# Kernel optimization log

Hardware: AMD Instinct MI355X
Metric: run time of the kernel (lower is better)

The kernel has to match this reference:

```python
import jax, jax.numpy as jnp
import numpy as np

# dims
B, W, L = 64, 64, 16          # sentences, words per sentence, max chars per word
E, H, V = 128, 512, 256       # char_embedding_size, word_embedding_size, char vocab


def setup_inputs() -> dict:
    key = jax.random.key(0)
    ks = jax.random.split(key, 8)
    chars = jax.random.randint(ks[0], (B, W, L), 1, V)          # char ids (0 = pad, unused in valid region)
    word_lens = jax.random.randint(ks[1], (B, W), 1, L + 1)     # per-word char counts in [1, L]
    emb = (jax.random.normal(ks[2], (V, E), jnp.float32) * 0.1).at[0].set(0.0)  # padding_idx=0 -> zero row

    def lstm_params(k):
        k1, k2, k3, k4 = jax.random.split(k, 4)
        s = 1.0 / np.sqrt(H)
        return (jax.random.uniform(k1, (4 * H, E), jnp.float32, -s, s),
                jax.random.uniform(k2, (4 * H, H), jnp.float32, -s, s),
                jax.random.uniform(k3, (4 * H,), jnp.float32, -s, s),
                jax.random.uniform(k4, (4 * H,), jnp.float32, -s, s))

    Wih_f, Whh_f, bih_f, bhh_f = lstm_params(ks[3])
    Wih_b, Whh_b, bih_b, bhh_b = lstm_params(ks[4])
    s = 1.0 / np.sqrt(2 * H)
    Wp = jax.random.uniform(ks[5], (H, 2 * H), jnp.float32, -s, s)
    bp = jax.random.uniform(ks[6], (H,), jnp.float32, -s, s)
    return dict(chars=chars, word_lens=word_lens, emb=emb,
                Wih_f=Wih_f, Whh_f=Whh_f, bih_f=bih_f, bhh_f=bhh_f,
                Wih_b=Wih_b, Whh_b=Whh_b, bih_b=bih_b, bhh_b=bhh_b,
                Wp=Wp, bp=bp)


def _lstm_last(x, lens, Wih, Whh, b):
    """Run a batched LSTM over x [N,L,E]; return hidden state at step lens-1 -> [N,H].
    PyTorch gate order: i, f, g, o."""
    N = x.shape[0]
    xw = jnp.einsum('nle,ge->nlg', x, Wih) + b  # [N, L, 4H], input projections precomputed

    def step(carry, xt):
        h, c = carry
        g = xt + h @ Whh.T
        i, f, gg, o = jnp.split(g, 4, axis=-1)
        c = jax.nn.sigmoid(f) * c + jax.nn.sigmoid(i) * jnp.tanh(gg)
        h = jax.nn.sigmoid(o) * jnp.tanh(c)
        return (h, c), h

    init = (jnp.zeros((N, H), x.dtype), jnp.zeros((N, H), x.dtype))
    _, hs = jax.lax.scan(step, init, jnp.swapaxes(xw, 0, 1))  # [L, N, H]
    hs = jnp.swapaxes(hs, 0, 1)                               # [N, L, H]
    idx = jnp.broadcast_to((lens - 1)[:, None, None], (N, 1, H))
    return jnp.take_along_axis(hs, idx, axis=1)[:, 0]


def reference(chars, word_lens, emb, Wih_f, Whh_f, bih_f, bhh_f,
              Wih_b, Whh_b, bih_b, bhh_b, Wp, bp):
    N = B * W
    lens = word_lens.reshape(N)
    x = emb[chars.reshape(N, L)]  # [N, L, E] char embeddings (dropout is identity in eval)

    # forward direction: hidden at last valid char (padded steps come after, don't matter)
    h_fwd = _lstm_last(x, lens, Wih_f, Whh_f, bih_f + bhh_f)

    # backward direction == forward LSTM over the length-aware reversed word,
    # taking hidden at step lens-1 (matches pack_sequence backward output at pos 0)
    t = jnp.arange(L)
    rev_idx = jnp.clip(lens[:, None] - 1 - t[None, :], 0, L - 1)  # [N, L]
    x_rev = jnp.take_along_axis(x, rev_idx[:, :, None], axis=1)
    h_bwd = _lstm_last(x_rev, lens, Wih_b, Whh_b, bih_b + bhh_b)

    concat = jnp.concatenate([h_bwd, h_fwd], axis=-1)  # torch order: (reverse, forward)
    out = concat @ Wp.T + bp                            # [N, H]
    return out.reshape(B, W, H)
```

## Files before the change

### kernel.cpp

```cpp
#include <hip/hip_runtime.h>

typedef unsigned short u16;
typedef __bf16 bf16x8 __attribute__((ext_vector_type(8)));
typedef float f32x4 __attribute__((ext_vector_type(4)));

#define NW 4096
#define HDIM 512
#define EDIM 128
#define G4 2048
#define LMAX 16
#define KREC 640

__device__ __forceinline__ u16 f2bf(float f) {
  unsigned u = __float_as_uint(f);
  u += 0x7FFFu + ((u >> 16) & 1u);
  return (u16)(u >> 16);
}

__device__ __forceinline__ float sigf(float x) { return 1.f / (1.f + __expf(-x)); }
__device__ __forceinline__ float tanha(float x) {
  float ax = fabsf(x);
  float e = __expf(2.f * ax);
  float t = 1.f - 2.f / (e + 1.f);
  return x < 0.f ? -t : t;
}

__device__ __forceinline__ void gload16(const void* g, void* l) {
  __builtin_amdgcn_global_load_lds((const __attribute__((address_space(1))) void*)g,
                                   (__attribute__((address_space(3))) void*)l, 16, 0, 0);
}

union V16 { int4 i; bf16x8 b; };
__device__ __forceinline__ bf16x8 ldfrag(const u16* p) {
  V16 v; v.i = *(const int4*)p; return v.b;
}

__global__ __launch_bounds__(256) void sort_kernel(
    const int* __restrict__ lens,
    int* __restrict__ perm, int* __restrict__ lens_s, int* __restrict__ nactive) {
  __shared__ int cnt[LMAX + 1];
  __shared__ int start[LMAX + 1];
  __shared__ int cursor[LMAX + 1];
  int tid = threadIdx.x;
  if (tid <= LMAX) cnt[tid] = 0;
  __syncthreads();
  for (int w = tid; w < NW; w += 256) atomicAdd(&cnt[lens[w]], 1);
  __syncthreads();
  if (tid == 0) {
    int acc = 0;
    for (int l = LMAX; l >= 1; --l) { start[l] = acc; acc += cnt[l]; }
    start[0] = acc;
  }
  __syncthreads();
  if (tid <= LMAX) cursor[tid] = start[tid];
  if (tid < LMAX) nactive[tid] = start[tid];
  __syncthreads();
  for (int w = tid; w < NW; w += 256) {
    int l = lens[w];
    int pos = atomicAdd(&cursor[l], 1);
    perm[pos] = w;
    lens_s[pos] = l;
  }
}

__global__ __launch_bounds__(256) void prep_kernel(
    const int* __restrict__ chars,
    const int* __restrict__ perm, const int* __restrict__ lens_s,
    const float* __restrict__ emb,
    const float* __restrict__ Wih_f, const float* __restrict__ Whh_f,
    const float* __restrict__ bih_f, const float* __restrict__ bhh_f,
    const float* __restrict__ Wih_b, const float* __restrict__ Whh_b,
    const float* __restrict__ bih_b, const float* __restrict__ bhh_b,
    const float* __restrict__ Wp,
    u16* __restrict__ Wcat, float* __restrict__ bcat, u16* __restrict__ Wpb,
    u16* __restrict__ Xf, u16* __restrict__ Xb) {
  int idx = blockIdx.x * 256 + threadIdx.x;
  if (idx < 327680) {
    int d = idx / (2048 * 80);
    int r = idx % (2048 * 80);
    int p = r / 80, c8 = r % 80;
    int unit = p >> 2, gate = p & 3;
    int orig = gate * 512 + unit;
    const float* Wih = d ? Wih_b : Wih_f;
    const float* Whh = d ? Whh_b : Whh_f;
    int k = c8 * 8;
    const float* src = (k < EDIM) ? (Wih + (size_t)orig * EDIM + k)
                                  : (Whh + (size_t)orig * HDIM + (k - EDIM));
    union { u16 u[8]; int4 v; } t;
#pragma unroll
    for (int j = 0; j < 8; ++j) t.u[j] = f2bf(src[j]);
    *(int4*)(Wcat + ((size_t)d * G4 + p) * KREC + k) = t.v;
  } else if (idx < 331776) {
    int r = idx - 327680;
    int d = r / G4, p = r % G4;
    int unit = p >> 2, gate = p & 3;
    int orig = gate * 512 + unit;
    bcat[d * G4 + p] = d ? (bih_b[orig] + bhh_b[orig]) : (bih_f[orig] + bhh_f[orig]);
  } else if (idx < 397312) {
    int r = idx - 331776;
    int row = r >> 7, c8 = r & 127;
    union { u16 u[8]; int4 v; } t;
#pragma unroll
    for (int j = 0; j < 8; ++j) t.u[j] = f2bf(Wp[(size_t)row * 1024 + c8 * 8 + j]);
    *(int4*)(Wpb + (size_t)row * 1024 + c8 * 8) = t.v;
  } else {
    int r = idx - 397312;
    int tw = r >> 4, e8 = (r & 15) * 8;
    int t = tw >> 12, s = tw & (NW - 1);
    int w = perm[s];
    int len = lens_s[s];
    int cf = chars[w * LMAX + t];
    int tb = len - 1 - t; if (tb < 0) tb = 0;
    int cb = chars[w * LMAX + tb];
    union { u16 u[8]; int4 v; } vf, vb;
#pragma unroll
    for (int j = 0; j < 8; ++j) {
      vf.u[j] = f2bf(emb[(size_t)cf * EDIM + e8 + j]);
      vb.u[j] = f2bf(emb[(size_t)cb * EDIM + e8 + j]);
    }
    size_t o = ((size_t)t * NW + s) * EDIM + e8;
    *(int4*)(Xf + o) = vf.v;
    *(int4*)(Xb + o) = vb.v;
  }
}

__global__ __launch_bounds__(256) void step_kernel(
    const u16* __restrict__ Wcat, const float* __restrict__ bcat,
    const u16* __restrict__ Xf, const u16* __restrict__ Xb,
    const u16* __restrict__ hprev, u16* __restrict__ hnext,
    float* __restrict__ cst, u16* __restrict__ concat,
    const int* __restrict__ perm, const int* __restrict__ lens_s,
    const int* __restrict__ nactive, int t, int nIter, int first) {
  const int w0 = blockIdx.x * 128;
  if (w0 >= nactive[t]) return;

  __shared__ u16 ldsA[128 * 64];
  __shared__ u16 ldsB[128 * 64];

  const int tid = threadIdx.x;
  const int lane = tid & 63;
  const int wid = tid >> 6;
  const int wm = wid >> 1, wn = wid & 1;
  const int dir = blockIdx.z;
  const int m0 = blockIdx.y * 128;

  const u16* Wd = Wcat + (size_t)dir * G4 * KREC;
  const u16* Xd = dir ? Xb : Xf;
  const u16* hpd = hprev + (size_t)dir * NW * HDIM;

  f32x4 acc[4][4];
#pragma unroll
  for (int i = 0; i < 4; ++i)
#pragma unroll
    for (int j = 0; j < 4; ++j) acc[i][j] = (f32x4){0.f, 0.f, 0.f, 0.f};

  const int srow = tid >> 3;
  const int c8 = tid & 7;

  for (int kit = 0; kit < nIter; ++kit) {
    const int k0 = kit * 64;
#pragma unroll
    for (int s = 0; s < 4; ++s) {
      int rr = s * 32 + srow;
      gload16(Wd + (size_t)(m0 + rr) * KREC + k0 + c8 * 8, ldsA + rr * 64 + c8 * 8);
    }
#pragma unroll
    for (int s = 0; s < 4; ++s) {
      int rr = s * 32 + srow;
      int word = w0 + rr;
      int k = k0 + c8 * 8;
      const u16* src = (k < EDIM) ? (Xd + ((size_t)t * NW + word) * EDIM + k)
                                  : (hpd + (size_t)word * HDIM + (k - EDIM));
      gload16(src, ldsB + rr * 64 + c8 * 8);
    }
    __syncthreads();
#pragma unroll
    for (int kk = 0; kk < 2; ++kk) {
      const int ko = kk * 32 + (lane >> 4) * 8;
      bf16x8 af[4], bfr[4];
#pragma unroll
      for (int mi = 0; mi < 4; ++mi)
        af[mi] = ldfrag(ldsA + (wm * 64 + mi * 16 + (lane & 15)) * 64 + ko);
#pragma unroll
      for (int ni = 0; ni < 4; ++ni)
        bfr[ni] = ldfrag(ldsB + (wn * 64 + ni * 16 + (lane & 15)) * 64 + ko);
#pragma unroll
      for (int mi = 0; mi < 4; ++mi)
#pragma unroll
        for (int ni = 0; ni < 4; ++ni)
          acc[mi][ni] = __builtin_amdgcn_mfma_f32_16x16x32_bf16(af[mi], bfr[ni], acc[mi][ni], 0, 0, 0);
    }
    __syncthreads();
  }

  const float* bcd = bcat + dir * G4;
  float* cd = cst + (size_t)dir * HDIM * NW;
  u16* hstage = ldsA;
#pragma unroll
  for (int mi = 0; mi < 4; ++mi) {
    int ul = wm * 16 + mi * 4 + (lane >> 4);
    int unit = blockIdx.y * 32 + ul;
    float4 bb = *(const float4*)(bcd + 4 * unit);
#pragma unroll
    for (int ni = 0; ni < 4; ++ni) {
      int wl = wn * 64 + ni * 16 + (lane & 15);
      int word = w0 + wl;
      f32x4 a = acc[mi][ni];
      float gi = a[0] + bb.x, gf = a[1] + bb.y, gg = a[2] + bb.z, go = a[3] + bb.w;
      size_t cidx = (size_t)unit * NW + word;
      float c0 = first ? 0.f : cd[cidx];
      float cn = sigf(gf) * c0 + sigf(gi) * tanha(gg);
      float hh = sigf(go) * tanha(cn);
      cd[cidx] = cn;
      hstage[wl * 32 + ul] = f2bf(hh);
    }
  }
  __syncthreads();

  u16* hnd = hnext + (size_t)dir * NW * HDIM;
  const int dirOff = dir ? 0 : HDIM;
#pragma unroll
  for (int r = 0; r < 2; ++r) {
    int i4 = tid * 2 + r;
    int wl = i4 >> 2, part = i4 & 3;
    int word = w0 + wl;
    int4 v = ((const int4*)hstage)[i4];
    *(int4*)(hnd + (size_t)word * HDIM + blockIdx.y * 32 + part * 8) = v;
    if (t == lens_s[word] - 1) {
      int orig = perm[word];
      *(int4*)(concat + (size_t)orig * 1024 + dirOff + blockIdx.y * 32 + part * 8) = v;
    }
  }
}

__global__ __launch_bounds__(256) void proj_kernel(
    const u16* __restrict__ concat, const u16* __restrict__ Wpb,
    const float* __restrict__ bp, float* __restrict__ out) {
  __shared__ u16 ldsA[128 * 64];
  __shared__ u16 ldsB[128 * 64];

  const int tid = threadIdx.x;
  const int lane = tid & 63;
  const int wid = tid >> 6;
  const int wm = wid >> 1, wn = wid & 1;
  const int m0 = blockIdx.x * 128;
  const int n0 = blockIdx.y * 128;

  f32x4 acc[4][4];
#pragma unroll
  for (int i = 0; i < 4; ++i)
#pragma unroll
    for (int j = 0; j < 4; ++j) acc[i][j] = (f32x4){0.f, 0.f, 0.f, 0.f};

  const int srow = tid >> 3;
  const int c8 = tid & 7;

  for (int kit = 0; kit < 16; ++kit) {
    const int k0 = kit * 64;
#pragma unroll
    for (int s = 0; s < 4; ++s) {
      int rr = s * 32 + srow;
      gload16(concat + (size_t)(m0 + rr) * 1024 + k0 + c8 * 8, ldsA + rr * 64 + c8 * 8);
      gload16(Wpb + (size_t)(n0 + rr) * 1024 + k0 + c8 * 8, ldsB + rr * 64 + c8 * 8);
    }
    __syncthreads();
#pragma unroll
    for (int kk = 0; kk < 2; ++kk) {
      const int ko = kk * 32 + (lane >> 4) * 8;
      bf16x8 af[4], bfr[4];
#pragma unroll
      for (int mi = 0; mi < 4; ++mi)
        af[mi] = ldfrag(ldsA + (wm * 64 + mi * 16 + (lane & 15)) * 64 + ko);
#pragma unroll
      for (int ni = 0; ni < 4; ++ni)
        bfr[ni] = ldfrag(ldsB + (wn * 64 + ni * 16 + (lane & 15)) * 64 + ko);
#pragma unroll
      for (int mi = 0; mi < 4; ++mi)
#pragma unroll
        for (int ni = 0; ni < 4; ++ni)
          acc[mi][ni] = __builtin_amdgcn_mfma_f32_16x16x32_bf16(af[mi], bfr[ni], acc[mi][ni], 0, 0, 0);
    }
    __syncthreads();
  }

  float bpv[4];
#pragma unroll
  for (int ni = 0; ni < 4; ++ni) bpv[ni] = bp[n0 + wn * 64 + ni * 16 + (lane & 15)];
#pragma unroll
  for (int mi = 0; mi < 4; ++mi)
#pragma unroll
    for (int ni = 0; ni < 4; ++ni)
#pragma unroll
      for (int rg = 0; rg < 4; ++rg) {
        int word = m0 + wm * 64 + mi * 16 + (lane >> 4) * 4 + rg;
        int hout = n0 + wn * 64 + ni * 16 + (lane & 15);
        out[(size_t)word * HDIM + hout] = acc[mi][ni][rg] + bpv[ni];
      }
}

extern "C" void kernel_launch(void* const* d_in, const int* in_sizes, int n_in,
                              void* d_out, int out_size, void* d_ws, size_t ws_size,
                              hipStream_t stream) {
  const int* chars = (const int*)d_in[0];
  const int* lens  = (const int*)d_in[1];
  const float* emb = (const float*)d_in[2];
  const float* Wih_f = (const float*)d_in[3];
  const float* Whh_f = (const float*)d_in[4];
  const float* bih_f = (const float*)d_in[5];
  const float* bhh_f = (const float*)d_in[6];
  const float* Wih_b = (const float*)d_in[7];
  const float* Whh_b = (const float*)d_in[8];
  const float* bih_b = (const float*)d_in[9];
  const float* bhh_b = (const float*)d_in[10];
  const float* Wp = (const float*)d_in[11];
  const float* bp = (const float*)d_in[12];
  float* out = (float*)d_out;

  char* ws = (char*)d_ws;
  size_t o = 0;
  u16* Wcat = (u16*)(ws + o);  o += (size_t)2 * G4 * KREC * 2;
  float* bcat = (float*)(ws + o); o += (size_t)2 * G4 * 4;
  u16* Wpb = (u16*)(ws + o);   o += (size_t)HDIM * 1024 * 2;
  u16* Xf = (u16*)(ws + o);    o += (size_t)LMAX * NW * EDIM * 2;
  u16* Xb = (u16*)(ws + o);    o += (size_t)LMAX * NW * EDIM * 2;
  u16* hbuf = (u16*)(ws + o);  o += (size_t)2 * 2 * NW * HDIM * 2;
  float* cst = (float*)(ws + o); o += (size_t)2 * HDIM * NW * 4;
  u16* concat = (u16*)(ws + o); o += (size_t)NW * 1024 * 2;
  int* perm = (int*)(ws + o);  o += (size_t)NW * 4;
  int* lens_s = (int*)(ws + o); o += (size_t)NW * 4;
  int* nactive = (int*)(ws + o); o += 64;

  sort_kernel<<<1, 256, 0, stream>>>(lens, perm, lens_s, nactive);

  prep_kernel<<<5648, 256, 0, stream>>>(chars, perm, lens_s, emb,
      Wih_f, Whh_f, bih_f, bhh_f, Wih_b, Whh_b, bih_b, bhh_b, Wp,
      Wcat, bcat, Wpb, Xf, Xb);

  const size_t hping = (size_t)2 * NW * HDIM;
  for (int t = 0; t < LMAX; ++t) {
    int ping = t & 1;
    u16* hprev = hbuf + (size_t)ping * hping;
    u16* hnext = hbuf + (size_t)(ping ^ 1) * hping;
    int nIter = (t == 0) ? 2 : 10;
    step_kernel<<<dim3(32, 16, 2), 256, 0, stream>>>(
        Wcat, bcat, Xf, Xb, hprev, hnext, cst, concat,
        perm, lens_s, nactive, t, nIter, t == 0 ? 1 : 0);
  }

  proj_kernel<<<dim3(32, 4), 256, 0, stream>>>(concat, Wpb, bp, out);
}
```

Measured before the change: 851.3 us.

## Swizzle global bf16 layouts for conflict-free LDS reads and double-buffer step GEMM

Weights, embeddings, hidden states and concat are now stored with an XOR swizzle of 16-byte chunks keyed on the row index. Because the direct-to-LDS copies preserve that order, the MFMA fragment reads from LDS hit different banks instead of conflicting. The step kernel also double-buffers its LDS tiles, so the next K-slice loads while the current one computes. This doubles LDS use per block and requires every producer and consumer of these buffers to agree on the swizzle.

```diff
diff --git a/kernel.cpp b/kernel.cpp
--- a/kernel.cpp
+++ b/kernel.cpp
@@ -89,7 +89,7 @@
     union { u16 u[8]; int4 v; } t;
 #pragma unroll
     for (int j = 0; j < 8; ++j) t.u[j] = f2bf(src[j]);
-    *(int4*)(Wcat + ((size_t)d * G4 + p) * KREC + k) = t.v;
+    *(int4*)(Wcat + ((size_t)d * G4 + p) * KREC + ((c8 ^ (p & 7)) * 8)) = t.v;
   } else if (idx < 331776) {
     int r = idx - 327680;
     int d = r / G4, p = r % G4;
@@ -102,11 +102,12 @@
     union { u16 u[8]; int4 v; } t;
 #pragma unroll
     for (int j = 0; j < 8; ++j) t.u[j] = f2bf(Wp[(size_t)row * 1024 + c8 * 8 + j]);
-    *(int4*)(Wpb + (size_t)row * 1024 + c8 * 8) = t.v;
+    *(int4*)(Wpb + (size_t)row * 1024 + ((c8 ^ (row & 7)) * 8)) = t.v;
   } else {
     int r = idx - 397312;
-    int tw = r >> 4, e8 = (r & 15) * 8;
+    int tw = r >> 4, l = r & 15;
     int t = tw >> 12, s = tw & (NW - 1);
+    int e8 = l * 8;
     int w = perm[s];
     int len = lens_s[s];
     int cf = chars[w * LMAX + t];
@@ -118,7 +119,7 @@
       vf.u[j] = f2bf(emb[(size_t)cf * EDIM + e8 + j]);
       vb.u[j] = f2bf(emb[(size_t)cb * EDIM + e8 + j]);
     }
-    size_t o = ((size_t)t * NW + s) * EDIM + e8;
+    size_t o = ((size_t)t * NW + s) * EDIM + ((l ^ (s & 7)) * 8);
     *(int4*)(Xf + o) = vf.v;
     *(int4*)(Xb + o) = vb.v;
   }
@@ -134,8 +135,8 @@
   const int w0 = blockIdx.x * 128;
   if (w0 >= nactive[t]) return;
 
-  __shared__ u16 ldsA[128 * 64];
-  __shared__ u16 ldsB[128 * 64];
+  __shared__ u16 ldsA[2][128 * 64];
+  __shared__ u16 ldsB[2][128 * 64];
 
   const int tid = threadIdx.x;
   const int lane = tid & 63;
@@ -157,12 +158,12 @@
   const int srow = tid >> 3;
   const int c8 = tid & 7;
 
-  for (int kit = 0; kit < nIter; ++kit) {
+  auto STAGE = [&](int buf, int kit) {
     const int k0 = kit * 64;
 #pragma unroll
     for (int s = 0; s < 4; ++s) {
       int rr = s * 32 + srow;
-      gload16(Wd + (size_t)(m0 + rr) * KREC + k0 + c8 * 8, ldsA + rr * 64 + c8 * 8);
+      gload16(Wd + (size_t)(m0 + rr) * KREC + k0 + c8 * 8, &ldsA[buf][rr * 64 + c8 * 8]);
     }
 #pragma unroll
     for (int s = 0; s < 4; ++s) {
@@ -171,31 +172,42 @@
       int k = k0 + c8 * 8;
       const u16* src = (k < EDIM) ? (Xd + ((size_t)t * NW + word) * EDIM + k)
                                   : (hpd + (size_t)word * HDIM + (k - EDIM));
-      gload16(src, ldsB + rr * 64 + c8 * 8);
-    }
-    __syncthreads();
+      gload16(src, &ldsB[buf][rr * 64 + c8 * 8]);
+    }
+  };
+
+  STAGE(0, 0);
+  asm volatile("s_waitcnt vmcnt(0)" ::: "memory");
+  __builtin_amdgcn_s_barrier();
+
+  const int key = lane & 7;
+  int cur = 0;
+  for (int kit = 0; kit < nIter; ++kit) {
+    if (kit + 1 < nIter) STAGE(cur ^ 1, kit + 1);
 #pragma unroll
     for (int kk = 0; kk < 2; ++kk) {
-      const int ko = kk * 32 + (lane >> 4) * 8;
+      const int pc = ((kk * 4 + (lane >> 4)) ^ key) * 8;
       bf16x8 af[4], bfr[4];
 #pragma unroll
       for (int mi = 0; mi < 4; ++mi)
-        af[mi] = ldfrag(ldsA + (wm * 64 + mi * 16 + (lane & 15)) * 64 + ko);
+        af[mi] = ldfrag(&ldsA[cur][(wm * 64 + mi * 16 + (lane & 15)) * 64 + pc]);
 #pragma unroll
       for (int ni = 0; ni < 4; ++ni)
-        bfr[ni] = ldfrag(ldsB + (wn * 64 + ni * 16 + (lane & 15)) * 64 + ko);
+        bfr[ni] = ldfrag(&ldsB[cur][(wn * 64 + ni * 16 + (lane & 15)) * 64 + pc]);
 #pragma unroll
       for (int mi = 0; mi < 4; ++mi)
 #pragma unroll
         for (int ni = 0; ni < 4; ++ni)
           acc[mi][ni] = __builtin_amdgcn_mfma_f32_16x16x32_bf16(af[mi], bfr[ni], acc[mi][ni], 0, 0, 0);
     }
-    __syncthreads();
+    asm volatile("s_waitcnt vmcnt(0)" ::: "memory");
+    __builtin_amdgcn_s_barrier();
+    cur ^= 1;
   }
 
   const float* bcd = bcat + dir * G4;
   float* cd = cst + (size_t)dir * HDIM * NW;
-  u16* hstage = ldsA;
+  u16* hstage = &ldsA[0][0];
 #pragma unroll
   for (int mi = 0; mi < 4; ++mi) {
     int ul = wm * 16 + mi * 4 + (lane >> 4);
@@ -218,17 +230,19 @@
   __syncthreads();
 
   u16* hnd = hnext + (size_t)dir * NW * HDIM;
-  const int dirOff = dir ? 0 : HDIM;
+  const int coff = dir ? 0 : 64;
 #pragma unroll
   for (int r = 0; r < 2; ++r) {
     int i4 = tid * 2 + r;
     int wl = i4 >> 2, part = i4 & 3;
     int word = w0 + wl;
     int4 v = ((const int4*)hstage)[i4];
-    *(int4*)(hnd + (size_t)word * HDIM + blockIdx.y * 32 + part * 8) = v;
+    int c2 = blockIdx.y * 4 + part;
+    *(int4*)(hnd + (size_t)word * HDIM + ((c2 ^ (word & 7)) * 8)) = v;
     if (t == lens_s[word] - 1) {
       int orig = perm[word];
-      *(int4*)(concat + (size_t)orig * 1024 + dirOff + blockIdx.y * 32 + part * 8) = v;
+      int cc = coff + blockIdx.y * 4 + part;
+      *(int4*)(concat + (size_t)orig * 1024 + ((cc ^ (orig & 7)) * 8)) = v;
     }
   }
 }
@@ -254,6 +268,7 @@
 
   const int srow = tid >> 3;
   const int c8 = tid & 7;
+  const int key = lane & 7;
 
   for (int kit = 0; kit < 16; ++kit) {
     const int k0 = kit * 64;
@@ -266,14 +281,14 @@
     __syncthreads();
 #pragma unroll
     for (int kk = 0; kk < 2; ++kk) {
-      const int ko = kk * 32 + (lane >> 4) * 8;
+      const int pc = ((kk * 4 + (lane >> 4)) ^ key) * 8;
       bf16x8 af[4], bfr[4];
 #pragma unroll
       for (int mi = 0; mi < 4; ++mi)
-        af[mi] = ldfrag(ldsA + (wm * 64 + mi * 16 + (lane & 15)) * 64 + ko);
+        af[mi] = ldfrag(ldsA + (wm * 64 + mi * 16 + (lane & 15)) * 64 + pc);
 #pragma unroll
       for (int ni = 0; ni < 4; ++ni)
-        bfr[ni] = ldfrag(ldsB + (wn * 64 + ni * 16 + (lane & 15)) * 64 + ko);
+        bfr[ni] = ldfrag(ldsB + (wn * 64 + ni * 16 + (lane & 15)) * 64 + pc);
 #pragma unroll
       for (int mi = 0; mi < 4; ++mi)
 #pragma unroll
```

Result: faster. 728.1 us (-14.5%).
